# Optimization experiments

Hardware: AMD Instinct MI355X
Metric: run time of the kernel (lower is better)

Reference implementation:

```python
import jax, jax.numpy as jnp
import numpy as np

D_MODEL = 768
N_HEAD = 12
D_FF = 3072
SEQ = 2048
BSZ = 4
EPS = 1e-5


def _linear_params(key, d_in, d_out):
    k1, k2 = jax.random.split(key)
    bound = 1.0 / np.sqrt(d_in)
    W = jax.random.uniform(k1, (d_in, d_out), jnp.float32, -bound, bound)
    b = jax.random.uniform(k2, (d_out,), jnp.float32, -bound, bound)
    return W, b


def setup_inputs() -> dict:
    key = jax.random.key(0)
    ks = jax.random.split(key, 8)
    src = jax.random.normal(ks[0], (SEQ, BSZ, D_MODEL), jnp.float32)
    Wq, bq = _linear_params(ks[1], D_MODEL, D_MODEL)
    Wk, bk = _linear_params(ks[2], D_MODEL, D_MODEL)
    Wv, bv = _linear_params(ks[3], D_MODEL, D_MODEL)
    Wo, bo = _linear_params(ks[4], D_MODEL, D_MODEL)
    W1, b1 = _linear_params(ks[5], D_MODEL, D_FF)
    W2, b2 = _linear_params(ks[6], D_FF, D_MODEL)
    g1 = jnp.ones((D_MODEL,), jnp.float32)
    be1 = jnp.zeros((D_MODEL,), jnp.float32)
    g2 = jnp.ones((D_MODEL,), jnp.float32)
    be2 = jnp.zeros((D_MODEL,), jnp.float32)
    return dict(src=src, Wq=Wq, bq=bq, Wk=Wk, bk=bk, Wv=Wv, bv=bv,
                Wo=Wo, bo=bo, W1=W1, b1=b1, W2=W2, b2=b2,
                g1=g1, be1=be1, g2=g2, be2=be2)


def _layer_norm(x, g, b):
    mu = jnp.mean(x, axis=-1, keepdims=True)
    var = jnp.mean(jnp.square(x - mu), axis=-1, keepdims=True)
    return (x - mu) * jax.lax.rsqrt(var + EPS) * g + b


def reference(src, Wq, bq, Wk, bk, Wv, bv, Wo, bo, W1, b1, W2, b2, g1, be1, g2, be2):
    L, B, D = src.shape
    H = N_HEAD
    hd = D // H
    # in-projection: (L,B,D) -> (B*H, L, hd)
    def split_heads(x):
        return x.reshape(L, B * H, hd).transpose(1, 0, 2)
    q = split_heads(src @ Wq + bq)
    k = split_heads(src @ Wk + bk)
    v = split_heads(src @ Wv + bv)
    # NOTE: original code applies NO 1/sqrt(head_dim) scaling
    scores = jnp.einsum('bqd,bkd->bqk', q, k)  # (B*H, L, L)
    attn = jax.nn.softmax(scores, axis=-1)
    attn_out = jnp.einsum('bqk,bkd->bqd', attn, v)  # (B*H, L, hd)
    # out-projection
    attn_out = attn_out.transpose(1, 0, 2).reshape(L, B, D)
    src2 = attn_out @ Wo + bo
    x = _layer_norm(src + src2, g1, be1)
    ff = jax.nn.gelu(x @ W1 + b1, approximate=False) @ W2 + b2
    return _layer_norm(x + ff, g2, be2)
```

## Files before the change

### kernel.cpp

```cpp
#include <hip/hip_runtime.h>
#include <math.h>

#define D_MODEL 768
#define N_HEAD  12
#define HD      64
#define D_FF    3072
#define SEQ     2048
#define BSZ     4
#define NROWS   (SEQ * BSZ)

typedef unsigned short u16;
typedef __attribute__((ext_vector_type(8))) short short8;
typedef __attribute__((ext_vector_type(4))) float float4v;

enum { FLAG_GELU = 1, FLAG_ABLK = 2, FLAG_CBBLK = 4 };

__device__ __forceinline__ float gelu_exact(float x) {
    return 0.5f * x * (1.0f + erff(x * 0.70710678118654752440f));
}
__device__ __forceinline__ u16 f2b(float f) {
    unsigned u = __builtin_bit_cast(unsigned, f);
    return (u16)((u + 0x7fffu + ((u >> 16) & 1u)) >> 16);
}
__device__ __forceinline__ float b2f(u16 x) {
    return __builtin_bit_cast(float, (unsigned)x << 16);
}
__device__ __forceinline__ void gll16(const u16* g, u16* l) {
    __builtin_amdgcn_global_load_lds(
        (const __attribute__((address_space(1))) unsigned*)g,
        (__attribute__((address_space(3))) unsigned*)l, 16, 0, 0);
}
__device__ __forceinline__ size_t blk_off(int row, int col, int k32) {
    return ((size_t)((row >> 7) * k32 + (col >> 5)) << 12)
         + ((row & 127) << 5) + (col & 31);
}

__global__ __launch_bounds__(256) void gemm_bt(
    const u16* __restrict__ A, int lda,
    const u16* __restrict__ Bt,
    const float* __restrict__ bias,
    const float* __restrict__ residf, const u16* __restrict__ residb, int ldr,
    float* __restrict__ Cf, u16* __restrict__ Cb, int ldc,
    int K, int flags)
{
    __shared__ u16 Ab[2][128 * 32];
    __shared__ u16 Bb[2][128 * 32];

    const int tid  = threadIdx.x;
    const int lane = tid & 63, wv = tid >> 6;
    const int row0 = blockIdx.x * 128, col0 = blockIdx.y * 128;
    const int mw = (wv & 1) * 64, nw = (wv >> 1) * 64;
    const int fr = lane & 15, fk = (lane >> 4) * 8;
    const int k32 = K >> 5;
    const int nIter = K >> 5;

    auto stage = [&](int buf, int k0) {
        const u16* baseB = Bt + (((size_t)(col0 >> 7) * k32 + (k0 >> 5)) << 12);
        if (flags & FLAG_ABLK) {
            const u16* baseA = A + (((size_t)(row0 >> 7) * k32 + (k0 >> 5)) << 12);
            #pragma unroll
            for (int i = 0; i < 2; ++i) {
                const int cid = i * 256 + wv * 64 + lane;
                gll16(baseA + (size_t)cid * 8, Ab[buf] + (size_t)cid * 8);
                gll16(baseB + (size_t)cid * 8, Bb[buf] + (size_t)cid * 8);
            }
        } else {
            #pragma unroll
            for (int i = 0; i < 2; ++i) {
                const int cid = i * 256 + wv * 64 + lane;
                const int r = cid >> 2, ch = (cid & 3) * 8;
                gll16(A + (size_t)(row0 + r) * lda + k0 + ch, Ab[buf] + (size_t)cid * 8);
                gll16(baseB + (size_t)cid * 8, Bb[buf] + (size_t)cid * 8);
            }
        }
    };

    float4v acc[4][4];
    #pragma unroll
    for (int i = 0; i < 4; ++i)
        #pragma unroll
        for (int j = 0; j < 4; ++j)
            acc[i][j] = float4v{0.f, 0.f, 0.f, 0.f};

    stage(0, 0);
    for (int it = 0; it < nIter; ++it) {
        const int cur = it & 1;
        __syncthreads();
        if (it + 1 < nIter) stage(cur ^ 1, (it + 1) * 32);

        short8 af[4], bfr[4];
        #pragma unroll
        for (int t = 0; t < 4; ++t) {
            af[t]  = *(const short8*)&Ab[cur][(mw + t * 16 + fr) * 32 + fk];
            bfr[t] = *(const short8*)&Bb[cur][(nw + t * 16 + fr) * 32 + fk];
        }
        #pragma unroll
        for (int mt = 0; mt < 4; ++mt)
            #pragma unroll
            for (int nt = 0; nt < 4; ++nt)
                acc[mt][nt] = __builtin_amdgcn_mfma_f32_16x16x32_bf16(
                    af[mt], bfr[nt], acc[mt][nt], 0, 0, 0);
    }

    #pragma unroll
    for (int mt = 0; mt < 4; ++mt)
        #pragma unroll
        for (int nt = 0; nt < 4; ++nt)
            #pragma unroll
            for (int r = 0; r < 4; ++r) {
                const int row = row0 + mw + mt * 16 + (lane >> 4) * 4 + r;
                const int col = col0 + nw + nt * 16 + fr;
                float v = acc[mt][nt][r];
                if (bias)              v += bias[col];
                if (flags & FLAG_GELU) v = gelu_exact(v);
                if (residf)            v += residf[(size_t)row * ldr + col];
                if (residb)            v += b2f(residb[blk_off(row, col, 24)]);
                if (Cf) Cf[(size_t)row * ldc + col] = v;
                if (Cb) Cb[(flags & FLAG_CBBLK) ? blk_off(row, col, ldc >> 5)
                                                : (size_t)row * ldc + col] = f2b(v);
            }
}

__global__ __launch_bounds__(256) void gemm_bt64(
    const u16* __restrict__ A, int lda,
    const u16* __restrict__ Bt,
    const float* __restrict__ bias,
    const float* __restrict__ residf, const u16* __restrict__ residb, int ldr,
    float* __restrict__ Cf, u16* __restrict__ Cb, int ldc,
    int K, int flags)
{
    __shared__ u16 Ab[2][128 * 32];
    __shared__ u16 Bb[2][64 * 32];

    const int tid  = threadIdx.x;
    const int lane = tid & 63, wv = tid >> 6;
    const int row0 = blockIdx.x * 128, col0 = blockIdx.y * 64;
    const int mw = wv * 32;
    const int fr = lane & 15, hi = lane >> 4, fk = hi * 8;
    const int k32 = K >> 5;
    const int nIter = K >> 5;

    auto stage = [&](int buf, int k0) {
        const u16* baseB = Bt + (((size_t)(col0 >> 7) * k32 + (k0 >> 5)) << 12)
                              + ((col0 & 64) << 5);
        gll16(baseB + (size_t)tid * 8, Bb[buf] + (size_t)tid * 8);
        if (flags & FLAG_ABLK) {
            const u16* baseA = A + (((size_t)(row0 >> 7) * k32 + (k0 >> 5)) << 12);
            #pragma unroll
            for (int i = 0; i < 2; ++i) {
                const int cid = i * 256 + tid;
                gll16(baseA + (size_t)cid * 8, Ab[buf] + (size_t)cid * 8);
            }
        } else {
            #pragma unroll
            for (int i = 0; i < 2; ++i) {
                const int cid = i * 256 + tid;
                const int r = cid >> 2, ch = (cid & 3) * 8;
                gll16(A + (size_t)(row0 + r) * lda + k0 + ch, Ab[buf] + (size_t)cid * 8);
            }
        }
    };

    float4v acc[2][4];
    #pragma unroll
    for (int i = 0; i < 2; ++i)
        #pragma unroll
        for (int j = 0; j < 4; ++j)
            acc[i][j] = float4v{0.f, 0.f, 0.f, 0.f};

    stage(0, 0);
    for (int it = 0; it < nIter; ++it) {
        const int cur = it & 1;
        __syncthreads();
        if (it + 1 < nIter) stage(cur ^ 1, (it + 1) * 32);

        short8 af[2], bfr[4];
        #pragma unroll
        for (int t = 0; t < 2; ++t)
            af[t] = *(const short8*)&Ab[cur][(mw + t * 16 + fr) * 32 + fk];
        #pragma unroll
        for (int t = 0; t < 4; ++t)
            bfr[t] = *(const short8*)&Bb[cur][(t * 16 + fr) * 32 + fk];
        #pragma unroll
        for (int mt = 0; mt < 2; ++mt)
            #pragma unroll
            for (int nt = 0; nt < 4; ++nt)
                acc[mt][nt] = __builtin_amdgcn_mfma_f32_16x16x32_bf16(
                    af[mt], bfr[nt], acc[mt][nt], 0, 0, 0);
    }

    #pragma unroll
    for (int mt = 0; mt < 2; ++mt)
        #pragma unroll
        for (int nt = 0; nt < 4; ++nt)
            #pragma unroll
            for (int r = 0; r < 4; ++r) {
                const int row = row0 + mw + mt * 16 + hi * 4 + r;
                const int col = col0 + nt * 16 + fr;
                float v = acc[mt][nt][r];
                if (bias)              v += bias[col];
                if (flags & FLAG_GELU) v = gelu_exact(v);
                if (residf)            v += residf[(size_t)row * ldr + col];
                if (residb)            v += b2f(residb[blk_off(row, col, 24)]);
                if (Cf) Cf[(size_t)row * ldc + col] = v;
                if (Cb) Cb[(flags & FLAG_CBBLK) ? blk_off(row, col, ldc >> 5)
                                                : (size_t)row * ldc + col] = f2b(v);
            }
}

__global__ __launch_bounds__(256) void vt_kernel(
    const u16* __restrict__ qkv, u16* __restrict__ vt)
{
    __shared__ u16 t[64][72];
    const int tid = threadIdx.x;
    const int bh = blockIdx.y, b = bh / N_HEAD, h = bh % N_HEAD;
    const int l0 = blockIdx.x * 64;
    #pragma unroll
    for (int p = 0; p < 2; ++p) {
        const int idx = p * 256 + tid;
        const int lr = idx >> 3, c8 = (idx & 7) * 8;
        const int ch = (idx & 7) ^ ((idx >> 6) & 7);
        *(short8*)&t[lr][ch * 8] = *(const short8*)
            &qkv[blk_off((l0 + lr) * BSZ + b, 1536 + h * 64 + c8, 72)];
    }
    __syncthreads();
    #pragma unroll
    for (int p = 0; p < 2; ++p) {
        const int idx = p * 256 + tid;
        const int dr = idx >> 3, l8 = (idx & 7) * 8;
        const int sc = (((dr >> 3) ^ (idx & 7)) << 3) + (dr & 7);
        short8 vv;
        #pragma unroll
        for (int j = 0; j < 8; ++j) vv[j] = (short)t[l8 + j][sc];
        *(short8*)&vt[((size_t)(bh * 64 + dr)) * SEQ + l0 + l8] = vv;
    }
}

__global__ __launch_bounds__(256) void attn_kernel(
    const u16* __restrict__ qkv, const u16* __restrict__ vt,
    u16* __restrict__ o)
{
    __shared__ u16 Kt[2][64 * 64];
    __shared__ u16 Vt[2][64 * 64];
    __shared__ u16 PQ[128 * 72];

    const int tid  = threadIdx.x;
    const int lane = tid & 63, wv = tid >> 6;
    const int fr = lane & 15, hi = lane >> 4;
    const int bh = blockIdx.x, b = bh / N_HEAD, h = bh % N_HEAD;
    const int q0 = blockIdx.y * 128;

    auto stageKV = [&](int buf, int kt) {
        #pragma unroll
        for (int i = 0; i < 2; ++i) {
            const int cid = i * 256 + wv * 64 + lane;
            const int r = cid >> 3, c = cid & 7;
            const int cs = (c ^ (r & 7)) * 8;
            gll16(qkv + blk_off((kt + r) * BSZ + b, 768 + h * 64 + cs, 72),
                  Kt[buf] + (size_t)cid * 8);
            gll16(vt + (size_t)(bh * 64 + r) * SEQ + kt + cs,
                  Vt[buf] + (size_t)cid * 8);
        }
    };

    #pragma unroll
    for (int i = 0; i < 4; ++i) {
        const int cid = i * 256 + wv * 64 + lane;
        const int r = cid >> 3, c = cid & 7;
        gll16(qkv + blk_off((q0 + r) * BSZ + b, h * 64 + ((c ^ (r & 7)) * 8), 72),
              PQ + (size_t)cid * 8);
    }
    stageKV(0, 0);
    __syncthreads();

    short8 qf[2][2];
    #pragma unroll
    for (int mt = 0; mt < 2; ++mt) {
        const int row = wv * 32 + mt * 16 + fr;
        #pragma unroll
        for (int kb = 0; kb < 2; ++kb)
            qf[mt][kb] = *(const short8*)&PQ[row * 64 + (((kb << 2) + hi) ^ (fr & 7)) * 8];
    }

    const short8 ones = {(short)0x3F80, (short)0x3F80, (short)0x3F80, (short)0x3F80,
                         (short)0x3F80, (short)0x3F80, (short)0x3F80, (short)0x3F80};
    float4v oacc[2][4], ls[2];
    #pragma unroll
    for (int mt = 0; mt < 2; ++mt) {
        ls[mt] = float4v{0.f, 0.f, 0.f, 0.f};
        #pragma unroll
        for (int nt = 0; nt < 4; ++nt) oacc[mt][nt] = float4v{0.f, 0.f, 0.f, 0.f};
    }

    for (int it = 0; it < SEQ / 64; ++it) {
        const int cur = it & 1;
        __syncthreads();
        if (it + 1 < SEQ / 64) stageKV(cur ^ 1, (it + 1) * 64);

        float4v s[2][4];
        #pragma unroll
        for (int mt = 0; mt < 2; ++mt)
            #pragma unroll
            for (int nt = 0; nt < 4; ++nt) s[mt][nt] = float4v{0.f, 0.f, 0.f, 0.f};
        #pragma unroll
        for (int kb = 0; kb < 2; ++kb) {
            short8 kfr[4];
            #pragma unroll
            for (int nt = 0; nt < 4; ++nt)
                kfr[nt] = *(const short8*)&Kt[cur][(nt * 16 + fr) * 64 + (((kb << 2) + hi) ^ (fr & 7)) * 8];
            #pragma unroll
            for (int mt = 0; mt < 2; ++mt)
                #pragma unroll
                for (int nt = 0; nt < 4; ++nt)
                    s[mt][nt] = __builtin_amdgcn_mfma_f32_16x16x32_bf16(
                        qf[mt][kb], kfr[nt], s[mt][nt], 0, 0, 0);
        }

        #pragma unroll
        for (int mt = 0; mt < 2; ++mt)
            #pragma unroll
            for (int nt = 0; nt < 4; ++nt)
                #pragma unroll
                for (int r = 0; r < 4; ++r)
                    PQ[(wv * 32 + mt * 16 + hi * 4 + r) * 72 + nt * 16 + fr]
                        = f2b(__expf(s[mt][nt][r] - 16.0f));

        #pragma unroll
        for (int kb = 0; kb < 2; ++kb) {
            short8 pf[2], vfr[4];
            #pragma unroll
            for (int mt = 0; mt < 2; ++mt)
                pf[mt] = *(const short8*)&PQ[(wv * 32 + mt * 16 + fr) * 72 + kb * 32 + hi * 8];
            #pragma unroll
            for (int nt = 0; nt < 4; ++nt)
                vfr[nt] = *(const short8*)&Vt[cur][(nt * 16 + fr) * 64 + (((kb << 2) + hi) ^ (fr & 7)) * 8];
            #pragma unroll
            for (int mt = 0; mt < 2; ++mt) {
                ls[mt] = __builtin_amdgcn_mfma_f32_16x16x32_bf16(pf[mt], ones, ls[mt], 0, 0, 0);
                #pragma unroll
                for (int nt = 0; nt < 4; ++nt)
                    oacc[mt][nt] = __builtin_amdgcn_mfma_f32_16x16x32_bf16(
                        pf[mt], vfr[nt], oacc[mt][nt], 0, 0, 0);
            }
        }
    }

    #pragma unroll
    for (int mt = 0; mt < 2; ++mt)
        #pragma unroll
        for (int r = 0; r < 4; ++r) {
            const int qr = wv * 32 + mt * 16 + hi * 4 + r;
            const float linv = 1.0f / ls[mt][r];
            #pragma unroll
            for (int nt = 0; nt < 4; ++nt)
                o[((size_t)(q0 + qr) * BSZ + b) * D_MODEL + h * 64 + nt * 16 + fr]
                    = f2b(oacc[mt][nt][r] * linv);
        }
}

__global__ __launch_bounds__(256) void ln_kernel(
    const float* __restrict__ x, float* __restrict__ outf, u16* __restrict__ outb,
    const float* __restrict__ g, const float* __restrict__ be)
{
    const int row = blockIdx.x;
    const int tid = threadIdx.x;
    const float* xr = x + (size_t)row * D_MODEL;
    float v[3];
    float s = 0.0f, sq = 0.0f;
    #pragma unroll
    for (int j = 0; j < 3; ++j) {
        v[j] = xr[tid + 256 * j];
        s  += v[j];
        sq += v[j] * v[j];
    }
    #pragma unroll
    for (int off = 32; off > 0; off >>= 1) {
        s  += __shfl_down(s, off);
        sq += __shfl_down(sq, off);
    }
    __shared__ float ws_[8], wq_[8];
    if ((tid & 63) == 0) { ws_[tid >> 6] = s; wq_[tid >> 6] = sq; }
    __syncthreads();
    if (tid == 0) {
        float S = 0.0f, Q = 0.0f;
        #pragma unroll
        for (int w = 0; w < 4; ++w) { S += ws_[w]; Q += wq_[w]; }
        ws_[4] = S; wq_[4] = Q;
    }
    __syncthreads();
    const float mu   = ws_[4] * (1.0f / D_MODEL);
    const float var  = wq_[4] * (1.0f / D_MODEL) - mu * mu;
    const float rstd = rsqrtf(var + 1e-5f);
    #pragma unroll
    for (int j = 0; j < 3; ++j) {
        const int c = tid + 256 * j;
        const float y = (v[j] - mu) * rstd * g[c] + be[c];
        if (outf) outf[(size_t)row * D_MODEL + c] = y;
        if (outb) outb[blk_off(row, c, 24)] = f2b(y);
    }
}

__device__ __forceinline__ void transpose_body(
    const float* __restrict__ in, u16* __restrict__ out, int R, int Cn,
    int bx, int by, int tid, float (*t)[33])
{
    const int c0 = bx * 32, r0 = by * 32;
    const int tx = tid & 31, ty = tid >> 5;
    #pragma unroll
    for (int i = 0; i < 4; ++i)
        t[ty + i * 8][tx] = in[(size_t)(r0 + ty + i * 8) * Cn + c0 + tx];
    __syncthreads();
    const int k32 = R >> 5;
    #pragma unroll
    for (int i = 0; i < 4; ++i)
        out[blk_off(c0 + ty + i * 8, r0 + tx, k32)] = f2b(t[tx][ty + i * 8]);
}

__global__ __launch_bounds__(256) void prep_kernel(
    const float* __restrict__ Wq, const float* __restrict__ Wk,
    const float* __restrict__ Wv, const float* __restrict__ Wo,
    const float* __restrict__ W1, const float* __restrict__ W2,
    const float* __restrict__ src,
    const float* __restrict__ bq, const float* __restrict__ bk,
    const float* __restrict__ bv,
    u16* __restrict__ WqkvT, u16* __restrict__ WoT,
    u16* __restrict__ W1T, u16* __restrict__ W2T,
    u16* __restrict__ srcb, float* __restrict__ bqkv)
{
    __shared__ float t[32][33];
    const int id = blockIdx.x, tid = threadIdx.x;
    if (id < 6912) {
        const float* tin; u16* tout; int R, Cn, bx, by;
        if (id < 2304) {
            const int z = id / 576, i = id - z * 576;
            tin  = (z == 0) ? Wq : (z == 1) ? Wk : (z == 2) ? Wv : Wo;
            tout = (z == 3) ? WoT : WqkvT + z * 768 * 768;
            R = 768; Cn = 768; bx = i % 24; by = i / 24;
        } else if (id < 4608) {
            const int i = id - 2304;
            tin = W1; tout = W1T; R = 768; Cn = 3072; bx = i % 96; by = i / 96;
        } else {
            const int i = id - 4608;
            tin = W2; tout = W2T; R = 3072; Cn = 768; bx = i % 24; by = i / 24;
        }
        transpose_body(tin, tout, R, Cn, bx, by, tid, t);
    } else if (id < 9984) {
        const int i = (id - 6912) * 256 + tid;
        const int row = i / 96;
        const int c8  = (i - row * 96) * 8;
        const float4 a = *(const float4*)&src[(size_t)row * 768 + c8];
        const float4 b = *(const float4*)&src[(size_t)row * 768 + c8 + 4];
        uint4 pk;
        pk.x = (unsigned)f2b(a.x) | ((unsigned)f2b(a.y) << 16);
        pk.y = (unsigned)f2b(a.z) | ((unsigned)f2b(a.w) << 16);
        pk.z = (unsigned)f2b(b.x) | ((unsigned)f2b(b.y) << 16);
        pk.w = (unsigned)f2b(b.z) | ((unsigned)f2b(b.w) << 16);
        *(uint4*)&srcb[blk_off(row, c8, 24)] = pk;
    } else {
        const int i = (id - 9984) * 256 + tid;
        if (i < 2304)
            bqkv[i] = (i < 768) ? bq[i] : (i < 1536) ? bk[i - 768] : bv[i - 1536];
    }
}

extern "C" void kernel_launch(void* const* d_in, const int* in_sizes, int n_in,
                              void* d_out, int out_size, void* d_ws, size_t ws_size,
                              hipStream_t stream)
{
    (void)in_sizes; (void)n_in; (void)out_size; (void)ws_size;
    const float* src = (const float*)d_in[0];
    const float* Wq  = (const float*)d_in[1];
    const float* bq  = (const float*)d_in[2];
    const float* Wk  = (const float*)d_in[3];
    const float* bk  = (const float*)d_in[4];
    const float* Wv  = (const float*)d_in[5];
    const float* bv  = (const float*)d_in[6];
    const float* Wo  = (const float*)d_in[7];
    const float* bo  = (const float*)d_in[8];
    const float* W1  = (const float*)d_in[9];
    const float* b1  = (const float*)d_in[10];
    const float* W2  = (const float*)d_in[11];
    const float* b2  = (const float*)d_in[12];
    const float* g1  = (const float*)d_in[13];
    const float* be1 = (const float*)d_in[14];
    const float* g2  = (const float*)d_in[15];
    const float* be2 = (const float*)d_in[16];
    float* out = (float*)d_out;

    char* w = (char*)d_ws;
    u16* WqkvT = (u16*)w; w += (size_t)2304 * 768 * 2;
    u16* WoT   = (u16*)w; w += (size_t)768 * 768 * 2;
    u16* W1T   = (u16*)w; w += (size_t)D_FF * 768 * 2;
    u16* W2T   = (u16*)w; w += (size_t)768 * D_FF * 2;
    float* bqkv = (float*)w; w += 2304 * 4 + 64;
    char* A0 = w; w += (size_t)NROWS * 768 * 2;
    char* A1 = w; w += (size_t)NROWS * 2304 * 2;
    char* A2 = w; w += (size_t)NROWS * 768 * 2;
    u16*   srcb  = (u16*)A0;
    u16*   vtb   = (u16*)A0;
    u16*   qkvb  = (u16*)A1;
    float* sum   = (float*)A1;
    u16*   attnb = (u16*)A2;
    u16*   x1b   = (u16*)A2;
    u16*   hb    = (u16*)A0;

    const dim3 blk(256);

    prep_kernel<<<dim3(9993), blk, 0, stream>>>(
        Wq, Wk, Wv, Wo, W1, W2, src, bq, bk, bv,
        WqkvT, WoT, W1T, W2T, srcb, bqkv);

    gemm_bt<<<dim3(64, 18), blk, 0, stream>>>(srcb, 0, WqkvT, bqkv,
        nullptr, nullptr, 0, nullptr, qkvb, 2304, 768, FLAG_ABLK | FLAG_CBBLK);

    vt_kernel<<<dim3(32, 48), blk, 0, stream>>>(qkvb, vtb);
    attn_kernel<<<dim3(BSZ * N_HEAD, SEQ / 128), blk, 0, stream>>>(qkvb, vtb, attnb);

    gemm_bt64<<<dim3(64, 12), blk, 0, stream>>>(attnb, 768, WoT, bo,
        src, nullptr, 768, sum, nullptr, 768, 768, 0);
    ln_kernel<<<dim3(NROWS), blk, 0, stream>>>(sum, nullptr, x1b, g1, be1);

    gemm_bt<<<dim3(64, 24), blk, 0, stream>>>(x1b, 0, W1T, b1,
        nullptr, nullptr, 0, nullptr, hb, 3072, 768, FLAG_GELU | FLAG_ABLK | FLAG_CBBLK);
    gemm_bt64<<<dim3(64, 12), blk, 0, stream>>>(hb, 0, W2T, b2,
        nullptr, x1b, 768, out, nullptr, 768, 3072, FLAG_ABLK);

    ln_kernel<<<dim3(NROWS), blk, 0, stream>>>(out, out, nullptr, g2, be2);
}
```

Baseline: 487.8 us.

## Use 256x128 GEMM tiles with 512 threads and XOR-swizzled LDS layout

Replaces the 128x128 GEMM used for the QKV and FFN1 projections with a 256x128-tile kernel running 8 waves per block, so each B tile is reused across twice as many rows. It also applies an XOR swizzle to the 16-byte chunks written into LDS (in both GEMM kernels) and matches it on the fragment reads, to reduce LDS bank conflicts. The wider tile doubles LDS use per block and halves the grid, which may lower occupancy and tail balance.

```diff
diff --git a/kernel.cpp b/kernel.cpp
--- a/kernel.cpp
+++ b/kernel.cpp
@@ -35,43 +35,40 @@
          + ((row & 127) << 5) + (col & 31);
 }
 
-__global__ __launch_bounds__(256) void gemm_bt(
-    const u16* __restrict__ A, int lda,
+__global__ __launch_bounds__(512) void gemm_bt256(
+    const u16* __restrict__ A,
     const u16* __restrict__ Bt,
     const float* __restrict__ bias,
-    const float* __restrict__ residf, const u16* __restrict__ residb, int ldr,
-    float* __restrict__ Cf, u16* __restrict__ Cb, int ldc,
+    u16* __restrict__ Cb, int ldc,
     int K, int flags)
 {
-    __shared__ u16 Ab[2][128 * 32];
+    __shared__ u16 Ab[2][256 * 32];
     __shared__ u16 Bb[2][128 * 32];
 
     const int tid  = threadIdx.x;
     const int lane = tid & 63, wv = tid >> 6;
-    const int row0 = blockIdx.x * 128, col0 = blockIdx.y * 128;
-    const int mw = (wv & 1) * 64, nw = (wv >> 1) * 64;
-    const int fr = lane & 15, fk = (lane >> 4) * 8;
+    const int row0 = blockIdx.x * 256, col0 = blockIdx.y * 128;
+    const int mw = (wv & 3) * 64, nw = (wv >> 2) * 64;
+    const int fr = lane & 15, hi = lane >> 4;
+    const int fk = (hi ^ ((fr >> 1) & 3)) * 8;
     const int k32 = K >> 5;
     const int nIter = K >> 5;
 
     auto stage = [&](int buf, int k0) {
         const u16* baseB = Bt + (((size_t)(col0 >> 7) * k32 + (k0 >> 5)) << 12);
-        if (flags & FLAG_ABLK) {
-            const u16* baseA = A + (((size_t)(row0 >> 7) * k32 + (k0 >> 5)) << 12);
-            #pragma unroll
-            for (int i = 0; i < 2; ++i) {
-                const int cid = i * 256 + wv * 64 + lane;
-                gll16(baseA + (size_t)cid * 8, Ab[buf] + (size_t)cid * 8);
-                gll16(baseB + (size_t)cid * 8, Bb[buf] + (size_t)cid * 8);
-            }
-        } else {
-            #pragma unroll
-            for (int i = 0; i < 2; ++i) {
-                const int cid = i * 256 + wv * 64 + lane;
-                const int r = cid >> 2, ch = (cid & 3) * 8;
-                gll16(A + (size_t)(row0 + r) * lda + k0 + ch, Ab[buf] + (size_t)cid * 8);
-                gll16(baseB + (size_t)cid * 8, Bb[buf] + (size_t)cid * 8);
-            }
+        {
+            const int r = tid >> 2;
+            const int sc = (((tid & 3) ^ ((r >> 1) & 3)) * 8);
+            gll16(baseB + (size_t)r * 32 + sc, Bb[buf] + (size_t)tid * 8);
+        }
+        #pragma unroll
+        for (int i = 0; i < 2; ++i) {
+            const int cid = i * 512 + tid;
+            const int r = cid >> 2;
+            const int sc = (((cid & 3) ^ ((r >> 1) & 3)) * 8);
+            const u16* baseA = A +
+                (((size_t)((row0 >> 7) + (r >> 7)) * k32 + (k0 >> 5)) << 12);
+            gll16(baseA + (size_t)(r & 127) * 32 + sc, Ab[buf] + (size_t)cid * 8);
         }
     };
 
@@ -108,16 +105,12 @@
         for (int nt = 0; nt < 4; ++nt)
             #pragma unroll
             for (int r = 0; r < 4; ++r) {
-                const int row = row0 + mw + mt * 16 + (lane >> 4) * 4 + r;
+                const int row = row0 + mw + mt * 16 + hi * 4 + r;
                 const int col = col0 + nw + nt * 16 + fr;
                 float v = acc[mt][nt][r];
                 if (bias)              v += bias[col];
                 if (flags & FLAG_GELU) v = gelu_exact(v);
-                if (residf)            v += residf[(size_t)row * ldr + col];
-                if (residb)            v += b2f(residb[blk_off(row, col, 24)]);
-                if (Cf) Cf[(size_t)row * ldc + col] = v;
-                if (Cb) Cb[(flags & FLAG_CBBLK) ? blk_off(row, col, ldc >> 5)
-                                                : (size_t)row * ldc + col] = f2b(v);
+                Cb[blk_off(row, col, ldc >> 5)] = f2b(v);
             }
 }
 
@@ -136,27 +129,35 @@
     const int lane = tid & 63, wv = tid >> 6;
     const int row0 = blockIdx.x * 128, col0 = blockIdx.y * 64;
     const int mw = wv * 32;
-    const int fr = lane & 15, hi = lane >> 4, fk = hi * 8;
+    const int fr = lane & 15, hi = lane >> 4;
+    const int fk = (hi ^ ((fr >> 1) & 3)) * 8;
     const int k32 = K >> 5;
     const int nIter = K >> 5;
 
     auto stage = [&](int buf, int k0) {
         const u16* baseB = Bt + (((size_t)(col0 >> 7) * k32 + (k0 >> 5)) << 12)
                               + ((col0 & 64) << 5);
-        gll16(baseB + (size_t)tid * 8, Bb[buf] + (size_t)tid * 8);
+        {
+            const int r = tid >> 2;
+            const int sc = (((tid & 3) ^ ((r >> 1) & 3)) * 8);
+            gll16(baseB + (size_t)r * 32 + sc, Bb[buf] + (size_t)tid * 8);
+        }
         if (flags & FLAG_ABLK) {
             const u16* baseA = A + (((size_t)(row0 >> 7) * k32 + (k0 >> 5)) << 12);
             #pragma unroll
             for (int i = 0; i < 2; ++i) {
                 const int cid = i * 256 + tid;
-                gll16(baseA + (size_t)cid * 8, Ab[buf] + (size_t)cid * 8);
+                const int r = cid >> 2;
+                const int sc = (((cid & 3) ^ ((r >> 1) & 3)) * 8);
+                gll16(baseA + (size_t)r * 32 + sc, Ab[buf] + (size_t)cid * 8);
             }
         } else {
             #pragma unroll
             for (int i = 0; i < 2; ++i) {
                 const int cid = i * 256 + tid;
-                const int r = cid >> 2, ch = (cid & 3) * 8;
-                gll16(A + (size_t)(row0 + r) * lda + k0 + ch, Ab[buf] + (size_t)cid * 8);
+                const int r = cid >> 2;
+                const int sc = (((cid & 3) ^ ((r >> 1) & 3)) * 8);
+                gll16(A + (size_t)(row0 + r) * lda + k0 + sc, Ab[buf] + (size_t)cid * 8);
             }
         }
     };
@@ -505,13 +506,14 @@
     u16*   hb    = (u16*)A0;
 
     const dim3 blk(256);
+    const dim3 blk512(512);
 
     prep_kernel<<<dim3(9993), blk, 0, stream>>>(
         Wq, Wk, Wv, Wo, W1, W2, src, bq, bk, bv,
         WqkvT, WoT, W1T, W2T, srcb, bqkv);
 
-    gemm_bt<<<dim3(64, 18), blk, 0, stream>>>(srcb, 0, WqkvT, bqkv,
-        nullptr, nullptr, 0, nullptr, qkvb, 2304, 768, FLAG_ABLK | FLAG_CBBLK);
+    gemm_bt256<<<dim3(32, 18), blk512, 0, stream>>>(srcb, WqkvT, bqkv,
+        qkvb, 2304, 768, FLAG_ABLK | FLAG_CBBLK);
 
     vt_kernel<<<dim3(32, 48), blk, 0, stream>>>(qkvb, vtb);
     attn_kernel<<<dim3(BSZ * N_HEAD, SEQ / 128), blk, 0, stream>>>(qkvb, vtb, attnb);
@@ -520,8 +522,8 @@
         src, nullptr, 768, sum, nullptr, 768, 768, 0);
     ln_kernel<<<dim3(NROWS), blk, 0, stream>>>(sum, nullptr, x1b, g1, be1);
 
-    gemm_bt<<<dim3(64, 24), blk, 0, stream>>>(x1b, 0, W1T, b1,
-        nullptr, nullptr, 0, nullptr, hb, 3072, 768, FLAG_GELU | FLAG_ABLK | FLAG_CBBLK);
+    gemm_bt256<<<dim3(32, 24), blk512, 0, stream>>>(x1b, W1T, b1,
+        hb, 3072, 768, FLAG_GELU | FLAG_ABLK | FLAG_CBBLK);
     gemm_bt64<<<dim3(64, 12), blk, 0, stream>>>(hb, 0, W2T, b2,
         nullptr, x1b, 768, out, nullptr, 768, 3072, FLAG_ABLK);
 
```

After: 467.4 us (median of 2 runs). 4.2% less time.
